# Performance work log

Hardware: AMD Instinct MI355X
Metric: run time of the kernel (lower is better)

## Reference

```python
import jax, jax.numpy as jnp
import numpy as np

L, N, E, H = 4096, 1, 1024, 16
DH = E // H
SCALE = DH ** -0.5


def setup_inputs() -> dict:
    key = jax.random.key(0)
    k1, k2, k3 = jax.random.split(key, 3)
    # xavier_uniform-ish scales for faithfulness of magnitude
    lim_qkv = (6.0 / (3 * E + E)) ** 0.5
    lim_out = (6.0 / (E + E)) ** 0.5
    x = jax.random.normal(k1, (L, N, E), dtype=jnp.float32)
    w_qkv = jax.random.uniform(k2, (3 * E, E), dtype=jnp.float32, minval=-lim_qkv, maxval=lim_qkv)
    w_out = jax.random.uniform(k3, (E, E), dtype=jnp.float32, minval=-lim_out, maxval=lim_out)
    return {"x": x, "w_qkv": w_qkv, "w_out": w_out}


def reference(x, w_qkv, w_out):
    # x: [L, N, E]
    qkv = jnp.einsum('lne,fe->lnf', x, w_qkv)          # [L, N, 3E]
    q, k, v = jnp.split(qkv, 3, axis=-1)               # each [L, N, E]

    def to_heads(t):
        # [L, N, E] -> [N*H, L, DH]
        return t.reshape(L, N * H, DH).transpose(1, 0, 2)

    q = to_heads(q) * SCALE
    k = to_heads(k)
    v = to_heads(v)
    attn = jnp.einsum('bld,bmd->blm', q, k)            # [N*H, L, L]
    attn = jax.nn.softmax(attn, axis=-1)
    out = jnp.einsum('blm,bmd->bld', attn, v)          # [N*H, L, DH]
    out = out.transpose(1, 0, 2).reshape(L, N, E)
    return jnp.einsum('lne,fe->lnf', out, w_out)       # [L, N, E]
```

## Files before the change

kernel.cpp:

```cpp
#include <hip/hip_runtime.h>
#include <hip/hip_bf16.h>
#include <stdint.h>

#define L_SEQ 4096
#define EMB   1024
#define NHEAD 16
#define DHEAD 64

#define SM_SCALE 0.18033688011112042f
#define SM_FIXED_MAX 12.0f

typedef __attribute__((ext_vector_type(8))) short short8;
typedef __attribute__((ext_vector_type(4))) short s16x4;
typedef __attribute__((ext_vector_type(4))) float f32x4;

struct Pack8 { f32x4 lo, hi; };

__device__ inline short f2bf(float f) {
  union { float f; unsigned u; } c; c.f = f;
  unsigned r = (c.u + 0x7fffu + ((c.u >> 16) & 1u)) >> 16;
  return (short)(unsigned short)r;
}
__device__ inline unsigned fbits(float f) {
  union { float f; unsigned u; } c; c.f = f; return c.u;
}
__device__ inline unsigned pack_trunc(float f0, float f1) {
#if __has_builtin(__builtin_amdgcn_perm)
  return __builtin_amdgcn_perm(fbits(f1), fbits(f0), 0x07060302u);
#else
  return (fbits(f0) >> 16) | (fbits(f1) & 0xffff0000u);
#endif
}

#if __has_builtin(__builtin_amdgcn_exp2f)
#define EXP2F(x) __builtin_amdgcn_exp2f(x)
#else
#define EXP2F(x) exp2f(x)
#endif

__device__ inline void pl16swap(unsigned &x, unsigned &y) {
#if __has_builtin(__builtin_amdgcn_permlane16_swap)
  auto r = __builtin_amdgcn_permlane16_swap(x, y, false, false);
  x = r[0]; y = r[1];
#else
  asm volatile("v_permlane16_swap_b32 %0, %1" : "+v"(x), "+v"(y));
#endif
}

__device__ inline short8 mk8(unsigned d0, unsigned d1, unsigned d2, unsigned d3) {
  union { unsigned u[4]; short8 s; } c;
  c.u[0] = d0; c.u[1] = d1; c.u[2] = d2; c.u[3] = d3;
  return c.s;
}

template<bool F32>
__device__ inline auto ld8(const void* p, size_t off) {
  if constexpr (F32) {
    const float* f = (const float*)p + off;
    Pack8 r; r.lo = *(const f32x4*)f; r.hi = *(const f32x4*)(f + 4);
    return r;
  } else {
    return *(const short8*)((const short*)p + off);
  }
}
__device__ inline short8 cvt8(Pack8 r) {
  short8 o;
#pragma unroll
  for (int j = 0; j < 4; ++j) { o[j] = f2bf(r.lo[j]); o[4 + j] = f2bf(r.hi[j]); }
  return o;
}
__device__ inline short8 cvt8(short8 r) { return r; }

#define MFMA16(a, b, c) __builtin_amdgcn_mfma_f32_16x16x32_bf16(a, b, c, 0, 0, 0)
#define FZERO ((f32x4){0.f, 0.f, 0.f, 0.f})

__device__ inline void stage16(const void* g, void* l) {
  __builtin_amdgcn_global_load_lds(
      (const __attribute__((address_space(1))) void*)g,
      (__attribute__((address_space(3))) void*)l, 16, 0, 0);
}

__global__ __launch_bounds__(256)
void conv_kernel(const float* __restrict__ in, short* __restrict__ out, int n) {
  int i = (blockIdx.x * 256 + threadIdx.x) * 8;
  if (i >= n) return;
  Pack8 r; r.lo = *(const f32x4*)(in + i); r.hi = *(const f32x4*)(in + i + 4);
  *(short8*)(out + i) = cvt8(r);
}

__global__ __launch_bounds__(256, 3)
void gemm_qkv_dma(const short* __restrict__ A, const short* __restrict__ B,
                  short* __restrict__ qb, short* __restrict__ kb,
                  short* __restrict__ vt) {
  __shared__ __align__(16) short At[128 * 32];
  __shared__ __align__(16) short Bt[128 * 32];

  const int tid  = threadIdx.x;
  const int lane = tid & 63;
  const int wave = tid >> 6;
  const int quad = lane >> 4;
  const int l15  = lane & 15;
  const int q8   = quad << 3;

  const int bm  = (blockIdx.x / 24) << 7;
  const int bn  = (blockIdx.x % 24) << 7;
  const int wr  = wave >> 1;
  const int wc  = wave & 1;

  const short* Ab = A + (size_t)bm * EMB;
  const short* Bb = B + (size_t)bn * EMB;

  f32x4 acc[4][4];
#pragma unroll
  for (int r = 0; r < 4; ++r)
#pragma unroll
    for (int c = 0; c < 4; ++c) acc[r][c] = FZERO;

  const int arow = (wr * 64 + l15) * 32 + q8;
  const int brow = (wc * 64 + l15) * 32 + q8;
  const int wbase = tid & ~63;

  for (int kt = 0; kt < 32; ++kt) {
    __syncthreads();
    const int k0 = kt << 5;
#pragma unroll
    for (int j = 0; j < 2; ++j) {
      const int s = j * 256 + tid;
      const int row = s >> 2, qc = (s & 3) << 3;
      stage16(Ab + (size_t)row * EMB + k0 + qc,
              At + (size_t)(j * 256 + wbase) * 8);
      stage16(Bb + (size_t)row * EMB + k0 + qc,
              Bt + (size_t)(j * 256 + wbase) * 8);
    }
    __syncthreads();

    short8 af[4], bf[4];
#pragma unroll
    for (int r = 0; r < 4; ++r) af[r] = *(const short8*)(At + arow + r * 512);
#pragma unroll
    for (int c = 0; c < 4; ++c) bf[c] = *(const short8*)(Bt + brow + c * 512);
#pragma unroll
    for (int r = 0; r < 4; ++r)
#pragma unroll
      for (int c = 0; c < 4; ++c)
        acc[r][c] = MFMA16(af[r], bf[c], acc[r][c]);
  }

  if (bn < 2048) {
    short* dst = (bn < 1024) ? qb : kb;
    const int bcol = (bn < 1024) ? bn : bn - 1024;
    const float cs = (bn < 1024) ? SM_SCALE : 1.0f;
#pragma unroll
    for (int r = 0; r < 4; ++r)
#pragma unroll
      for (int c = 0; c < 4; ++c) {
        const int col = bcol + wc * 64 + c * 16 + l15;
#pragma unroll
        for (int reg = 0; reg < 4; ++reg) {
          const int row = bm + wr * 64 + r * 16 + quad * 4 + reg;
          dst[(size_t)row * EMB + col] = f2bf(acc[r][c][reg] * cs);
        }
      }
  } else {
    const int bcol = bn - 2048;
#pragma unroll
    for (int r = 0; r < 4; ++r)
#pragma unroll
      for (int c = 0; c < 4; ++c) {
        const int col  = bcol + wc * 64 + c * 16 + l15;
        const int rowb = bm + wr * 64 + r * 16 + quad * 4;
        s16x4 pk;
#pragma unroll
        for (int reg = 0; reg < 4; ++reg) pk[reg] = f2bf(acc[r][c][reg]);
        *(s16x4*)(vt + (size_t)col * L_SEQ + rowb) = pk;
      }
  }
}

__global__ __launch_bounds__(256, 3)
void gemm_qkv_f32(const short* __restrict__ A, const float* __restrict__ B,
                  short* __restrict__ qb, short* __restrict__ kb,
                  short* __restrict__ vt) {
  __shared__ __align__(16) short At[128 * 40];
  __shared__ __align__(16) short Bt[128 * 40];

  const int tid  = threadIdx.x;
  const int lane = tid & 63;
  const int wave = tid >> 6;
  const int quad = lane >> 4;
  const int l15  = lane & 15;
  const int q8   = quad << 3;

  const int bm  = (blockIdx.x / 24) << 7;
  const int bn  = (blockIdx.x % 24) << 7;
  const int wr  = wave >> 1;
  const int wc  = wave & 1;

  const int s0 = tid, s1 = tid + 256;
  const int ar0 = s0 >> 2, ac0 = (s0 & 3) << 3;
  const int ar1 = s1 >> 2, ac1 = (s1 & 3) << 3;

  const size_t aoff0 = (size_t)(bm + ar0) * EMB + ac0;
  const size_t aoff1 = (size_t)(bm + ar1) * EMB + ac1;
  const size_t boff0 = (size_t)(bn + ar0) * EMB + ac0;
  const size_t boff1 = (size_t)(bn + ar1) * EMB + ac1;

  f32x4 acc[4][4];
#pragma unroll
  for (int r = 0; r < 4; ++r)
#pragma unroll
    for (int c = 0; c < 4; ++c) acc[r][c] = FZERO;

  short8 ga0 = *(const short8*)(A + aoff0);
  short8 ga1 = *(const short8*)(A + aoff1);
  Pack8  gb0 = ld8<true>(B, boff0);
  Pack8  gb1 = ld8<true>(B, boff1);

  const int arow = (wr * 64 + l15) * 40 + q8;
  const int brow = (wc * 64 + l15) * 40 + q8;

  for (int kt = 0; kt < 32; ++kt) {
    __syncthreads();
    *(short8*)(At + ar0 * 40 + ac0) = ga0;
    *(short8*)(At + ar1 * 40 + ac1) = ga1;
    *(short8*)(Bt + ar0 * 40 + ac0) = cvt8(gb0);
    *(short8*)(Bt + ar1 * 40 + ac1) = cvt8(gb1);
    __syncthreads();

    if (kt + 1 < 32) {
      const size_t k0 = (size_t)(kt + 1) << 5;
      ga0 = *(const short8*)(A + aoff0 + k0);
      ga1 = *(const short8*)(A + aoff1 + k0);
      gb0 = ld8<true>(B, boff0 + k0);
      gb1 = ld8<true>(B, boff1 + k0);
    }

    short8 af[4], bf[4];
#pragma unroll
    for (int r = 0; r < 4; ++r) af[r] = *(const short8*)(At + arow + r * 640);
#pragma unroll
    for (int c = 0; c < 4; ++c) bf[c] = *(const short8*)(Bt + brow + c * 640);
#pragma unroll
    for (int r = 0; r < 4; ++r)
#pragma unroll
      for (int c = 0; c < 4; ++c)
        acc[r][c] = MFMA16(af[r], bf[c], acc[r][c]);
  }

  if (bn < 2048) {
    short* dst = (bn < 1024) ? qb : kb;
    const int bcol = (bn < 1024) ? bn : bn - 1024;
    const float cs = (bn < 1024) ? SM_SCALE : 1.0f;
#pragma unroll
    for (int r = 0; r < 4; ++r)
#pragma unroll
      for (int c = 0; c < 4; ++c) {
        const int col = bcol + wc * 64 + c * 16 + l15;
#pragma unroll
        for (int reg = 0; reg < 4; ++reg) {
          const int row = bm + wr * 64 + r * 16 + quad * 4 + reg;
          dst[(size_t)row * EMB + col] = f2bf(acc[r][c][reg] * cs);
        }
      }
  } else {
    const int bcol = bn - 2048;
#pragma unroll
    for (int r = 0; r < 4; ++r)
#pragma unroll
      for (int c = 0; c < 4; ++c) {
        const int col  = bcol + wc * 64 + c * 16 + l15;
        const int rowb = bm + wr * 64 + r * 16 + quad * 4;
        s16x4 pk;
#pragma unroll
        for (int reg = 0; reg < 4; ++reg) pk[reg] = f2bf(acc[r][c][reg]);
        *(s16x4*)(vt + (size_t)col * L_SEQ + rowb) = pk;
      }
  }
}

__global__ __launch_bounds__(256, 3)
void gemm_out_dma(const short* __restrict__ A, const short* __restrict__ B,
                  float* __restrict__ C) {
  __shared__ __align__(16) short At[128 * 32];
  __shared__ __align__(16) short Bt[64 * 32];

  const int tid  = threadIdx.x;
  const int lane = tid & 63;
  const int wave = tid >> 6;
  const int quad = lane >> 4;
  const int l15  = lane & 15;
  const int q8   = quad << 3;

  const int bm  = (blockIdx.x >> 4) << 7;
  const int bn  = (blockIdx.x & 15) << 6;
  const int wr  = wave >> 1;
  const int wc  = wave & 1;

  const short* Ab = A + (size_t)bm * EMB;
  const short* Bb = B + (size_t)bn * EMB;

  f32x4 acc[4][2];
#pragma unroll
  for (int r = 0; r < 4; ++r)
#pragma unroll
    for (int c = 0; c < 2; ++c) acc[r][c] = FZERO;

  const int arow = (wr * 64 + l15) * 32 + q8;
  const int brow = (wc * 32 + l15) * 32 + q8;
  const int wbase = tid & ~63;

  for (int kt = 0; kt < 32; ++kt) {
    __syncthreads();
    const int k0 = kt << 5;
#pragma unroll
    for (int j = 0; j < 2; ++j) {
      const int s = j * 256 + tid;
      const int row = s >> 2, qc = (s & 3) << 3;
      stage16(Ab + (size_t)row * EMB + k0 + qc,
              At + (size_t)(j * 256 + wbase) * 8);
    }
    {
      const int row = tid >> 2, qc = (tid & 3) << 3;
      stage16(Bb + (size_t)row * EMB + k0 + qc, Bt + (size_t)wbase * 8);
    }
    __syncthreads();

    short8 af[4], bf[2];
#pragma unroll
    for (int r = 0; r < 4; ++r) af[r] = *(const short8*)(At + arow + r * 512);
#pragma unroll
    for (int c = 0; c < 2; ++c) bf[c] = *(const short8*)(Bt + brow + c * 512);
#pragma unroll
    for (int r = 0; r < 4; ++r)
#pragma unroll
      for (int c = 0; c < 2; ++c)
        acc[r][c] = MFMA16(af[r], bf[c], acc[r][c]);
  }

#pragma unroll
  for (int r = 0; r < 4; ++r) {
#pragma unroll
    for (int c = 0; c < 2; ++c) {
      const int col = bn + wc * 32 + c * 16 + l15;
#pragma unroll
      for (int reg = 0; reg < 4; ++reg) {
        const int row = bm + wr * 64 + r * 16 + quad * 4 + reg;
        C[(size_t)row * EMB + col] = acc[r][c][reg];
      }
    }
  }
}

__global__ __launch_bounds__(256, 2)
void attn_kernel(short* __restrict__ qo, const short* __restrict__ kbuf,
                 const short* __restrict__ vtbuf) {
  __shared__ __align__(16) short SH[4][128 * 64];

  const int tid  = threadIdx.x;
  const int lane = tid & 63;
  const int w    = tid >> 6;
  const int quad = lane >> 4;
  const int l15  = lane & 15;
  const int q8   = quad << 3;
  const int vb8  = ((quad & 1) << 1) | (quad >> 1);

  const int h    = blockIdx.x >> 5;
  const int qblk = blockIdx.x & 31;
  const int hcol = h * 64;

  short8 qf[2][2];
#pragma unroll
  for (int g = 0; g < 2; ++g) {
    const short* qp = qo + (size_t)(qblk * 128 + w * 32 + g * 16 + l15) * EMB + hcol;
    qf[g][0] = *(const short8*)(qp + q8);
    qf[g][1] = *(const short8*)(qp + 32 + q8);
  }

  const short8 vone = {0x3F80, 0x3F80, 0x3F80, 0x3F80,
                       0x3F80, 0x3F80, 0x3F80, 0x3F80};

  f32x4 o[2][4];
#pragma unroll
  for (int g = 0; g < 2; ++g)
#pragma unroll
    for (int f = 0; f < 4; ++f) o[g][f] = FZERO;
  f32x4 l_c[2] = {FZERO, FZERO};

  const int kr0  = tid >> 3;
  const int klc8 = ((tid & 7) ^ (kr0 & 7)) << 3;
  const int vr0  = tid >> 4;
  const int vlc8 = ((tid & 15) ^ vr0) << 3;
  const short* kp = kbuf + (size_t)kr0 * EMB + hcol + klc8;
  const short* vp = vtbuf + (size_t)(hcol + vr0) * L_SEQ + vlc8;
  const int db = (tid & ~63) * 8;

  const int sx7 = (l15 & 7) << 3;
  const int pk0 = q8 ^ sx7, pk1 = pk0 ^ 32;

#pragma unroll
  for (int jj = 0; jj < 4; ++jj) {
    stage16(kp + (size_t)jj * 32 * EMB,  &SH[0][0] + jj * 2048 + db);
    stage16(vp + (size_t)jj * 16 * L_SEQ, &SH[2][0] + jj * 2048 + db);
  }

  for (int t = 0; t < 32; ++t) {
    short* const ktb = &SH[t & 1][0];
    short* const vtb = &SH[2 + (t & 1)][0];

    __syncthreads();

    if (t < 31) {
      const short* kpt = kp + (size_t)(t + 1) * 128 * EMB;
      const short* vpt = vp + (size_t)(t + 1) * 128;
      short* const kd = &SH[(t + 1) & 1][0];
      short* const vd = &SH[2 + ((t + 1) & 1)][0];
#pragma unroll
      for (int jj = 0; jj < 4; ++jj) {
        stage16(kpt + (size_t)jj * 32 * EMB,  kd + jj * 2048 + db);
        stage16(vpt + (size_t)jj * 16 * L_SEQ, vd + jj * 2048 + db);
      }
    }

#pragma unroll
    for (int j = 0; j < 4; ++j) {
      const int kra = (j * 32 + l15) * 64;
      const int krb = (j * 32 + 16 + l15) * 64;
      short8 kf0a = *(const short8*)(ktb + kra + pk0);
      short8 kf0b = *(const short8*)(ktb + kra + pk1);
      short8 kf1a = *(const short8*)(ktb + krb + pk0);
      short8 kf1b = *(const short8*)(ktb + krb + pk1);

      f32x4 s[2][2];
      s[0][0] = MFMA16(kf0a, qf[0][0], FZERO);
      s[0][0] = MFMA16(kf0b, qf[0][1], s[0][0]);
      s[0][1] = MFMA16(kf1a, qf[0][0], FZERO);
      s[0][1] = MFMA16(kf1b, qf[0][1], s[0][1]);
      s[1][0] = MFMA16(kf0a, qf[1][0], FZERO);
      s[1][0] = MFMA16(kf0b, qf[1][1], s[1][0]);
      s[1][1] = MFMA16(kf1a, qf[1][0], FZERO);
      s[1][1] = MFMA16(kf1b, qf[1][1], s[1][1]);

      short8 pa[2];
#pragma unroll
      for (int g = 0; g < 2; ++g) {
        float p[2][4];
#pragma unroll
        for (int i = 0; i < 2; ++i)
#pragma unroll
          for (int r = 0; r < 4; ++r)
            p[i][r] = EXP2F(s[g][i][r] - SM_FIXED_MAX);

        unsigned pk[2][2];
#pragma unroll
        for (int i = 0; i < 2; ++i) {
          pk[i][0] = pack_trunc(p[i][0], p[i][1]);
          pk[i][1] = pack_trunc(p[i][2], p[i][3]);
        }
        pl16swap(pk[0][0], pk[1][0]);
        pl16swap(pk[0][1], pk[1][1]);
        pa[g] = mk8(pk[0][0], pk[0][1], pk[1][0], pk[1][1]);

        f32x4 rsv = MFMA16(pa[g], vone, FZERO);
#pragma unroll
        for (int r = 0; r < 4; ++r) l_c[g][r] += rsv[r];
      }

#pragma unroll
      for (int fd = 0; fd < 4; ++fd) {
        const int vrow = (fd * 16 + l15) * 128;
        const int pc   = (((j << 2) | vb8) ^ l15) << 3;
        short8 vf = *(const short8*)(vtb + vrow + pc);
        o[0][fd] = MFMA16(pa[0], vf, o[0][fd]);
        o[1][fd] = MFMA16(pa[1], vf, o[1][fd]);
      }
    }
  }

  __syncthreads();
  short* const pw = &SH[0][0] + w * (32 * 72);
#pragma unroll
  for (int g = 0; g < 2; ++g) {
    f32x4 inv;
#pragma unroll
    for (int r = 0; r < 4; ++r) inv[r] = 1.0f / l_c[g][r];
    short* const pg = pw + g * (16 * 72);
#pragma unroll
    for (int f = 0; f < 4; ++f)
#pragma unroll
      for (int r = 0; r < 4; ++r)
        pg[(quad * 4 + r) * 72 + f * 16 + l15] = f2bf(o[g][f][r] * inv[r]);
  }

#pragma unroll
  for (int rr = 0; rr < 4; ++rr) {
    const int row = (lane >> 3) + rr * 8;
    const int c8  = (lane & 7) << 3;
    short8 gv = *(const short8*)(pw + row * 72 + c8);
    *(short8*)(qo + (size_t)(qblk * 128 + w * 32 + row) * EMB + hcol + c8) = gv;
  }
}

extern "C" void kernel_launch(void* const* d_in, const int* in_sizes, int n_in,
                              void* d_out, int out_size, void* d_ws, size_t ws_size,
                              hipStream_t stream) {
  (void)in_sizes; (void)n_in; (void)out_size;
  const float* x     = (const float*)d_in[0];
  const float* w_qkv = (const float*)d_in[1];
  const float* w_out = (const float*)d_in[2];

  short* qbuf  = (short*)d_ws;
  short* x_bf  = qbuf + (size_t)L_SEQ * EMB;
  short* wo_bf = x_bf;
  short* wq_bf = x_bf + (size_t)L_SEQ * EMB;
  short* kbuf  = (short*)d_out;
  short* vtbuf = kbuf + (size_t)L_SEQ * EMB;
  float* outp  = (float*)d_out;

  const bool big_ws = ws_size >= (size_t)24 * 1024 * 1024;

  conv_kernel<<<dim3(L_SEQ * EMB / 2048), 256, 0, stream>>>(x, x_bf, L_SEQ * EMB);
  if (big_ws)
    conv_kernel<<<dim3(3 * EMB * EMB / 2048), 256, 0, stream>>>(w_qkv, wq_bf, 3 * EMB * EMB);

  if (big_ws)
    gemm_qkv_dma<<<dim3(768), 256, 0, stream>>>(x_bf, wq_bf, qbuf, kbuf, vtbuf);
  else
    gemm_qkv_f32<<<dim3(768), 256, 0, stream>>>(x_bf, w_qkv, qbuf, kbuf, vtbuf);

  conv_kernel<<<dim3(EMB * EMB / 2048), 256, 0, stream>>>(w_out, wo_bf, EMB * EMB);

  attn_kernel<<<dim3(NHEAD * (L_SEQ / 128)), 256, 0, stream>>>(qbuf, kbuf, vtbuf);

  gemm_out_dma<<<dim3(512), 256, 0, stream>>>(qbuf, wo_bf, outp);
}
```

Before: 211.8 us.

## Double GEMM K-tile to 64 with XOR-swizzled LDS and merge conversion kernels

Both bf16 GEMMs (QKV projection and output projection) now stage a 64-wide K slice per iteration instead of 32. That halves the number of loop iterations and barrier pairs, and the DMA-to-LDS loads use an XOR swizzle to avoid bank conflicts on the fragment reads. The three fp32-to-bf16 conversions (x, w_qkv, w_out) are merged into one launch, with w_out given its own workspace slot so it can be converted up front. The trade-offs are more LDS per block, which may reduce occupancy, and a larger workspace requirement.

```diff
diff --git a/kernel.cpp b/kernel.cpp
--- a/kernel.cpp
+++ b/kernel.cpp
@@ -88,12 +88,125 @@
   *(short8*)(out + i) = cvt8(r);
 }
 
+__global__ __launch_bounds__(256)
+void conv3_kernel(const float* __restrict__ x, short* __restrict__ xb,
+                  const float* __restrict__ wq, short* __restrict__ wqb,
+                  const float* __restrict__ wo, short* __restrict__ wob) {
+  const int b = blockIdx.x;
+  const float* src; short* dst; int base;
+  if (b < 2048)      { src = x;  dst = xb;  base = b * 2048; }
+  else if (b < 3584) { src = wq; dst = wqb; base = (b - 2048) * 2048; }
+  else               { src = wo; dst = wob; base = (b - 3584) * 2048; }
+  const int i = base + threadIdx.x * 8;
+  Pack8 r; r.lo = *(const f32x4*)(src + i); r.hi = *(const f32x4*)(src + i + 4);
+  *(short8*)(dst + i) = cvt8(r);
+}
+
 __global__ __launch_bounds__(256, 3)
 void gemm_qkv_dma(const short* __restrict__ A, const short* __restrict__ B,
                   short* __restrict__ qb, short* __restrict__ kb,
                   short* __restrict__ vt) {
-  __shared__ __align__(16) short At[128 * 32];
-  __shared__ __align__(16) short Bt[128 * 32];
+  __shared__ __align__(16) short At[128 * 64];
+  __shared__ __align__(16) short Bt[128 * 64];
+
+  const int tid  = threadIdx.x;
+  const int lane = tid & 63;
+  const int wave = tid >> 6;
+  const int quad = lane >> 4;
+  const int l15  = lane & 15;
+
+  const int bm  = (blockIdx.x / 24) << 7;
+  const int bn  = (blockIdx.x % 24) << 7;
+  const int wr  = wave >> 1;
+  const int wc  = wave & 1;
+
+  const short* Ab = A + (size_t)bm * EMB;
+  const short* Bb = B + (size_t)bn * EMB;
+
+  f32x4 acc[4][4];
+#pragma unroll
+  for (int r = 0; r < 4; ++r)
+#pragma unroll
+    for (int c = 0; c < 4; ++c) acc[r][c] = FZERO;
+
+  const int srow = tid >> 3;
+  const int lc8  = ((tid & 7) ^ (srow & 7)) << 3;
+  const int wbase = tid & ~63;
+
+  const int pc0 = (quad ^ (l15 & 7)) << 3;
+  const int pc1 = pc0 ^ 32;
+  const int arow = (wr * 64 + l15) * 64;
+  const int brow = (wc * 64 + l15) * 64;
+
+  for (int kt = 0; kt < 16; ++kt) {
+    __syncthreads();
+    const int k0 = kt << 6;
+#pragma unroll
+    for (int j = 0; j < 4; ++j) {
+      stage16(Ab + (size_t)(j * 32 + srow) * EMB + k0 + lc8,
+              At + (size_t)(j * 256 + wbase) * 8);
+      stage16(Bb + (size_t)(j * 32 + srow) * EMB + k0 + lc8,
+              Bt + (size_t)(j * 256 + wbase) * 8);
+    }
+    __syncthreads();
+
+#pragma unroll
+    for (int kh = 0; kh < 2; ++kh) {
+      const int pc = kh ? pc1 : pc0;
+      short8 af[4], bf[4];
+#pragma unroll
+      for (int r = 0; r < 4; ++r)
+        af[r] = *(const short8*)(At + arow + r * 1024 + pc);
+#pragma unroll
+      for (int c = 0; c < 4; ++c)
+        bf[c] = *(const short8*)(Bt + brow + c * 1024 + pc);
+#pragma unroll
+      for (int r = 0; r < 4; ++r)
+#pragma unroll
+        for (int c = 0; c < 4; ++c)
+          acc[r][c] = MFMA16(af[r], bf[c], acc[r][c]);
+    }
+  }
+
+  const int q8 = quad << 3;
+  (void)q8;
+  if (bn < 2048) {
+    short* dst = (bn < 1024) ? qb : kb;
+    const int bcol = (bn < 1024) ? bn : bn - 1024;
+    const float cs = (bn < 1024) ? SM_SCALE : 1.0f;
+#pragma unroll
+    for (int r = 0; r < 4; ++r)
+#pragma unroll
+      for (int c = 0; c < 4; ++c) {
+        const int col = bcol + wc * 64 + c * 16 + l15;
+#pragma unroll
+        for (int reg = 0; reg < 4; ++reg) {
+          const int row = bm + wr * 64 + r * 16 + quad * 4 + reg;
+          dst[(size_t)row * EMB + col] = f2bf(acc[r][c][reg] * cs);
+        }
+      }
+  } else {
+    const int bcol = bn - 2048;
+#pragma unroll
+    for (int r = 0; r < 4; ++r)
+#pragma unroll
+      for (int c = 0; c < 4; ++c) {
+        const int col  = bcol + wc * 64 + c * 16 + l15;
+        const int rowb = bm + wr * 64 + r * 16 + quad * 4;
+        s16x4 pk;
+#pragma unroll
+        for (int reg = 0; reg < 4; ++reg) pk[reg] = f2bf(acc[r][c][reg]);
+        *(s16x4*)(vt + (size_t)col * L_SEQ + rowb) = pk;
+      }
+  }
+}
+
+__global__ __launch_bounds__(256, 3)
+void gemm_qkv_f32(const short* __restrict__ A, const float* __restrict__ B,
+                  short* __restrict__ qb, short* __restrict__ kb,
+                  short* __restrict__ vt) {
+  __shared__ __align__(16) short At[128 * 40];
+  __shared__ __align__(16) short Bt[128 * 40];
 
   const int tid  = threadIdx.x;
   const int lane = tid & 63;
@@ -107,95 +220,6 @@
   const int wr  = wave >> 1;
   const int wc  = wave & 1;
 
-  const short* Ab = A + (size_t)bm * EMB;
-  const short* Bb = B + (size_t)bn * EMB;
-
-  f32x4 acc[4][4];
-#pragma unroll
-  for (int r = 0; r < 4; ++r)
-#pragma unroll
-    for (int c = 0; c < 4; ++c) acc[r][c] = FZERO;
-
-  const int arow = (wr * 64 + l15) * 32 + q8;
-  const int brow = (wc * 64 + l15) * 32 + q8;
-  const int wbase = tid & ~63;
-
-  for (int kt = 0; kt < 32; ++kt) {
-    __syncthreads();
-    const int k0 = kt << 5;
-#pragma unroll
-    for (int j = 0; j < 2; ++j) {
-      const int s = j * 256 + tid;
-      const int row = s >> 2, qc = (s & 3) << 3;
-      stage16(Ab + (size_t)row * EMB + k0 + qc,
-              At + (size_t)(j * 256 + wbase) * 8);
-      stage16(Bb + (size_t)row * EMB + k0 + qc,
-              Bt + (size_t)(j * 256 + wbase) * 8);
-    }
-    __syncthreads();
-
-    short8 af[4], bf[4];
-#pragma unroll
-    for (int r = 0; r < 4; ++r) af[r] = *(const short8*)(At + arow + r * 512);
-#pragma unroll
-    for (int c = 0; c < 4; ++c) bf[c] = *(const short8*)(Bt + brow + c * 512);
-#pragma unroll
-    for (int r = 0; r < 4; ++r)
-#pragma unroll
-      for (int c = 0; c < 4; ++c)
-        acc[r][c] = MFMA16(af[r], bf[c], acc[r][c]);
-  }
-
-  if (bn < 2048) {
-    short* dst = (bn < 1024) ? qb : kb;
-    const int bcol = (bn < 1024) ? bn : bn - 1024;
-    const float cs = (bn < 1024) ? SM_SCALE : 1.0f;
-#pragma unroll
-    for (int r = 0; r < 4; ++r)
-#pragma unroll
-      for (int c = 0; c < 4; ++c) {
-        const int col = bcol + wc * 64 + c * 16 + l15;
-#pragma unroll
-        for (int reg = 0; reg < 4; ++reg) {
-          const int row = bm + wr * 64 + r * 16 + quad * 4 + reg;
-          dst[(size_t)row * EMB + col] = f2bf(acc[r][c][reg] * cs);
-        }
-      }
-  } else {
-    const int bcol = bn - 2048;
-#pragma unroll
-    for (int r = 0; r < 4; ++r)
-#pragma unroll
-      for (int c = 0; c < 4; ++c) {
-        const int col  = bcol + wc * 64 + c * 16 + l15;
-        const int rowb = bm + wr * 64 + r * 16 + quad * 4;
-        s16x4 pk;
-#pragma unroll
-        for (int reg = 0; reg < 4; ++reg) pk[reg] = f2bf(acc[r][c][reg]);
-        *(s16x4*)(vt + (size_t)col * L_SEQ + rowb) = pk;
-      }
-  }
-}
-
-__global__ __launch_bounds__(256, 3)
-void gemm_qkv_f32(const short* __restrict__ A, const float* __restrict__ B,
-                  short* __restrict__ qb, short* __restrict__ kb,
-                  short* __restrict__ vt) {
-  __shared__ __align__(16) short At[128 * 40];
-  __shared__ __align__(16) short Bt[128 * 40];
-
-  const int tid  = threadIdx.x;
-  const int lane = tid & 63;
-  const int wave = tid >> 6;
-  const int quad = lane >> 4;
-  const int l15  = lane & 15;
-  const int q8   = quad << 3;
-
-  const int bm  = (blockIdx.x / 24) << 7;
-  const int bn  = (blockIdx.x % 24) << 7;
-  const int wr  = wave >> 1;
-  const int wc  = wave & 1;
-
   const int s0 = tid, s1 = tid + 256;
   const int ar0 = s0 >> 2, ac0 = (s0 & 3) << 3;
   const int ar1 = s1 >> 2, ac1 = (s1 & 3) << 3;
@@ -281,15 +305,14 @@
 __global__ __launch_bounds__(256, 3)
 void gemm_out_dma(const short* __restrict__ A, const short* __restrict__ B,
                   float* __restrict__ C) {
-  __shared__ __align__(16) short At[128 * 32];
-  __shared__ __align__(16) short Bt[64 * 32];
+  __shared__ __align__(16) short At[128 * 64];
+  __shared__ __align__(16) short Bt[64 * 64];
 
   const int tid  = threadIdx.x;
   const int lane = tid & 63;
   const int wave = tid >> 6;
   const int quad = lane >> 4;
   const int l15  = lane & 15;
-  const int q8   = quad << 3;
 
   const int bm  = (blockIdx.x >> 4) << 7;
   const int bn  = (blockIdx.x & 15) << 6;
@@ -305,36 +328,44 @@
 #pragma unroll
     for (int c = 0; c < 2; ++c) acc[r][c] = FZERO;
 
-  const int arow = (wr * 64 + l15) * 32 + q8;
-  const int brow = (wc * 32 + l15) * 32 + q8;
+  const int srow = tid >> 3;
+  const int lc8  = ((tid & 7) ^ (srow & 7)) << 3;
   const int wbase = tid & ~63;
 
-  for (int kt = 0; kt < 32; ++kt) {
-    __syncthreads();
-    const int k0 = kt << 5;
-#pragma unroll
-    for (int j = 0; j < 2; ++j) {
-      const int s = j * 256 + tid;
-      const int row = s >> 2, qc = (s & 3) << 3;
-      stage16(Ab + (size_t)row * EMB + k0 + qc,
+  const int pc0 = (quad ^ (l15 & 7)) << 3;
+  const int pc1 = pc0 ^ 32;
+  const int arow = (wr * 64 + l15) * 64;
+  const int brow = (wc * 32 + l15) * 64;
+
+  for (int kt = 0; kt < 16; ++kt) {
+    __syncthreads();
+    const int k0 = kt << 6;
+#pragma unroll
+    for (int j = 0; j < 4; ++j)
+      stage16(Ab + (size_t)(j * 32 + srow) * EMB + k0 + lc8,
               At + (size_t)(j * 256 + wbase) * 8);
-    }
-    {
-      const int row = tid >> 2, qc = (tid & 3) << 3;
-      stage16(Bb + (size_t)row * EMB + k0 + qc, Bt + (size_t)wbase * 8);
-    }
-    __syncthreads();
-
-    short8 af[4], bf[2];
-#pragma unroll
-    for (int r = 0; r < 4; ++r) af[r] = *(const short8*)(At + arow + r * 512);
-#pragma unroll
-    for (int c = 0; c < 2; ++c) bf[c] = *(const short8*)(Bt + brow + c * 512);
-#pragma unroll
-    for (int r = 0; r < 4; ++r)
+#pragma unroll
+    for (int j = 0; j < 2; ++j)
+      stage16(Bb + (size_t)(j * 32 + srow) * EMB + k0 + lc8,
+              Bt + (size_t)(j * 256 + wbase) * 8);
+    __syncthreads();
+
+#pragma unroll
+    for (int kh = 0; kh < 2; ++kh) {
+      const int pc = kh ? pc1 : pc0;
+      short8 af[4], bf[2];
+#pragma unroll
+      for (int r = 0; r < 4; ++r)
+        af[r] = *(const short8*)(At + arow + r * 1024 + pc);
 #pragma unroll
       for (int c = 0; c < 2; ++c)
-        acc[r][c] = MFMA16(af[r], bf[c], acc[r][c]);
+        bf[c] = *(const short8*)(Bt + brow + c * 1024 + pc);
+#pragma unroll
+      for (int r = 0; r < 4; ++r)
+#pragma unroll
+        for (int c = 0; c < 2; ++c)
+          acc[r][c] = MFMA16(af[r], bf[c], acc[r][c]);
+    }
   }
 
 #pragma unroll
@@ -510,26 +541,25 @@
 
   short* qbuf  = (short*)d_ws;
   short* x_bf  = qbuf + (size_t)L_SEQ * EMB;
-  short* wo_bf = x_bf;
   short* wq_bf = x_bf + (size_t)L_SEQ * EMB;
+  short* wo_bf = wq_bf + (size_t)3 * EMB * EMB;
   short* kbuf  = (short*)d_out;
   short* vtbuf = kbuf + (size_t)L_SEQ * EMB;
   float* outp  = (float*)d_out;
 
   const bool big_ws = ws_size >= (size_t)24 * 1024 * 1024;
 
-  conv_kernel<<<dim3(L_SEQ * EMB / 2048), 256, 0, stream>>>(x, x_bf, L_SEQ * EMB);
-  if (big_ws)
-    conv_kernel<<<dim3(3 * EMB * EMB / 2048), 256, 0, stream>>>(w_qkv, wq_bf, 3 * EMB * EMB);
-
-  if (big_ws)
+  if (big_ws) {
+    conv3_kernel<<<dim3(4096), 256, 0, stream>>>(x, x_bf, w_qkv, wq_bf, w_out, wo_bf);
     gemm_qkv_dma<<<dim3(768), 256, 0, stream>>>(x_bf, wq_bf, qbuf, kbuf, vtbuf);
-  else
+    attn_kernel<<<dim3(NHEAD * (L_SEQ / 128)), 256, 0, stream>>>(qbuf, kbuf, vtbuf);
+    gemm_out_dma<<<dim3(512), 256, 0, stream>>>(qbuf, wo_bf, outp);
+  } else {
+    short* wo_small = x_bf;
+    conv_kernel<<<dim3(L_SEQ * EMB / 2048), 256, 0, stream>>>(x, x_bf, L_SEQ * EMB);
     gemm_qkv_f32<<<dim3(768), 256, 0, stream>>>(x_bf, w_qkv, qbuf, kbuf, vtbuf);
-
-  conv_kernel<<<dim3(EMB * EMB / 2048), 256, 0, stream>>>(w_out, wo_bf, EMB * EMB);
-
-  attn_kernel<<<dim3(NHEAD * (L_SEQ / 128)), 256, 0, stream>>>(qbuf, kbuf, vtbuf);
-
-  gemm_out_dma<<<dim3(512), 256, 0, stream>>>(qbuf, wo_bf, outp);
-}
+    conv_kernel<<<dim3(EMB * EMB / 2048), 256, 0, stream>>>(w_out, wo_small, EMB * EMB);
+    attn_kernel<<<dim3(NHEAD * (L_SEQ / 128)), 256, 0, stream>>>(qbuf, kbuf, vtbuf);
+    gemm_out_dma<<<dim3(512), 256, 0, stream>>>(qbuf, wo_small, outp);
+  }
+}
```

New measurement: 198.4 us. 1.07x faster.
